# Performance work log

Measured on AMD Instinct MI355X. Metric: run time of the kernel, lower is better.

The kernel has to match this reference:

```python
import math
import jax, jax.numpy as jnp
import numpy as np

B, T, C = 4, 2048, 1024
NH, HD = 16, 64  # n_head, head_dim
RANK = 128


def setup_inputs() -> dict:
    key = jax.random.key(0)
    ks = jax.random.split(key, 9)
    s_in = 1.0 / math.sqrt(C)
    s_r = 1.0 / math.sqrt(RANK)
    inp = {"x": jax.random.normal(ks[0], (B, T, C), dtype=jnp.float32)}
    for i, name in enumerate(["q", "k", "v", "c"]):
        inp[name + "A"] = jax.random.normal(ks[1 + 2 * i], (RANK, C), dtype=jnp.float32) * s_in
        inp[name + "B"] = jax.random.normal(ks[2 + 2 * i], (C, RANK), dtype=jnp.float32) * s_r
    return inp


def _lowrank(x, A, Bf):
    # HarmonicLinear: rank-r factorized linear, W = Bf @ A, y = x @ W^T
    return (x @ A.T) @ Bf.T


def reference(x, qA, qB, kA, kB, vA, vB, cA, cB):
    b, t, c = x.shape
    q = _lowrank(x, qA, qB).reshape(b, t, NH, HD).transpose(0, 2, 1, 3)  # [b,h,t,d]
    k = _lowrank(x, kA, kB).reshape(b, t, NH, HD).transpose(0, 2, 1, 3)
    v = _lowrank(x, vA, vB).reshape(b, t, NH, HD).transpose(0, 2, 1, 3)
    att = jnp.einsum("bhqd,bhkd->bhqk", q, k) * (1.0 / math.sqrt(HD))
    causal = jnp.tril(jnp.ones((t, t), dtype=bool))
    att = jnp.where(causal, att, -jnp.inf)
    att = jax.nn.softmax(att, axis=-1)
    y = jnp.einsum("bhqk,bhkd->bhqd", att, v)
    y = y.transpose(0, 2, 1, 3).reshape(b, t, c)
    return _lowrank(y, cA, cB)
```

## Files before the change

kernel.cpp:

```cpp
#include <hip/hip_runtime.h>

typedef unsigned short u16;
typedef __attribute__((ext_vector_type(8))) short bf16x8;
typedef __attribute__((ext_vector_type(4))) float f32x4;
typedef __attribute__((ext_vector_type(16))) float f32x16;
typedef __attribute__((ext_vector_type(4))) int i32x4;

typedef const __attribute__((address_space(1))) void gvoid_t;
typedef __attribute__((address_space(3))) void svoid_t;

__device__ __forceinline__ u16 f2bf(float f) {
  unsigned u = __builtin_bit_cast(unsigned, f);
  u += 0x7fffu + ((u >> 16) & 1u);
  return (u16)(u >> 16);
}

__device__ __forceinline__ unsigned cvtpk(float a, float b) {
  unsigned r;
  asm("v_cvt_pk_bf16_f32 %0, %1, %2" : "=v"(r) : "v"(a), "v"(b));
  return r;
}

__device__ __forceinline__ void gload_lds16(const u16* g, u16* ldsbase) {
  __builtin_amdgcn_global_load_lds((gvoid_t*)g, (svoid_t*)ldsbase, 16, 0, 0);
}

__device__ __forceinline__ void mfma16(f32x4& d, bf16x8 a, bf16x8 b) {
  asm("v_mfma_f32_16x16x32_bf16 %0, %1, %2, %0" : "+v"(d) : "v"(a), "v"(b));
}
__device__ __forceinline__ void mfma32(f32x16& d, bf16x8 a, bf16x8 b) {
  asm("v_mfma_f32_32x32x16_bf16 %0, %1, %2, %0" : "+v"(d) : "v"(a), "v"(b));
}
__device__ __forceinline__ void mfma_fence4(f32x4& a, f32x4& b, f32x4& c, f32x4& d) {
  asm volatile("s_nop 7\n\ts_nop 7" : "+v"(a), "+v"(b), "+v"(c), "+v"(d));
}
__device__ __forceinline__ void fence16x2(f32x16& a, f32x16& b) {
  asm volatile("s_nop 7\n\ts_nop 7\n\ts_nop 7" : "+v"(a), "+v"(b));
}

struct W8 { const float* s[8]; };
__global__ __launch_bounds__(256) void cvt_all_kernel(const float* __restrict__ x,
                                                      W8 w, u16* __restrict__ xb,
                                                      u16* __restrict__ wb) {
  const int b = blockIdx.x;
  const float* src;
  u16* dst;
  int i;
  if (b < 8192) {
    src = x; dst = xb;
    i = (b * 256 + (int)threadIdx.x) * 4;
  } else {
    const int wi = (b - 8192) >> 7;
    const int wo = (b - 8192) & 127;
    src = w.s[wi]; dst = wb + (size_t)wi * 131072;
    i = (wo * 256 + (int)threadIdx.x) * 4;
  }
  float4 v = *(const float4*)(src + i);
  ushort4 o = {f2bf(v.x), f2bf(v.y), f2bf(v.z), f2bf(v.w)};
  *(ushort4*)(dst + i) = o;
}

struct G3 { const u16* A[3]; const u16* B[3]; void* C[3]; float osc[3]; int vt[3]; };

template <typename OutT, int BM>
__global__ __launch_bounds__(256) void gemm_nt(G3 g, int M, int N, int K) {
  constexpr int NI = (BM == 128) ? 4 : 2;
  __shared__ __align__(16) u16 At[2][BM * 64];
  __shared__ __align__(16) u16 Bt[2][128 * 64];
  const int z = blockIdx.z;
  const u16* __restrict__ A = g.A[z];
  const u16* __restrict__ Bw = g.B[z];
  const float osc = g.osc[z];
  const int tid = threadIdx.x;
  const int lane = tid & 63, w = tid >> 6;
  const int wm = (BM == 128) ? (w >> 1) : 0;
  const int wn = (BM == 128) ? (w & 1) : w;
  constexpr int WNW = (BM == 128) ? 64 : 32;
  const int l15 = lane & 15, l4 = lane >> 4;
  const int row0 = blockIdx.x * BM, col0 = blockIdx.y * 128;
  const int srow = lane >> 3;
  const int schunk = ((lane & 7) ^ srow) * 8;
  const u16* Ag = A + (size_t)(row0 + w * 8 + srow) * K + schunk;
  const u16* Bg = Bw + (size_t)(col0 + w * 8 + srow) * K + schunk;
  f32x4 acc[4][NI] = {};
  auto STAGE = [&](int k0, int buf) {
#pragma unroll
    for (int i = 0; i < BM / 32; ++i)
      gload_lds16(Ag + (size_t)i * 32 * K + k0, &At[buf][(w * 8 + i * 32) * 64]);
#pragma unroll
    for (int i = 0; i < 4; ++i)
      gload_lds16(Bg + (size_t)i * 32 * K + k0, &Bt[buf][(w * 8 + i * 32) * 64]);
  };
  STAGE(0, 0);
  asm volatile("s_waitcnt vmcnt(0)" ::: "memory");
  __syncthreads();
  const int nk = K >> 6;
  for (int t = 0; t < nk; ++t) {
    const int cur = t & 1;
    if (t + 1 < nk) STAGE((t + 1) << 6, cur ^ 1);
#pragma unroll
    for (int kk = 0; kk < 64; kk += 32) {
      bf16x8 af[4], bfr[NI];
#pragma unroll
      for (int mi = 0; mi < 4; ++mi) {
        const int r = wm * 64 + mi * 16 + l15;
        af[mi] = *(const bf16x8*)&At[cur][r * 64 + ((kk + 8 * l4) ^ ((r & 7) << 3))];
      }
#pragma unroll
      for (int ni = 0; ni < NI; ++ni) {
        const int r = wn * WNW + ni * 16 + l15;
        bfr[ni] = *(const bf16x8*)&Bt[cur][r * 64 + ((kk + 8 * l4) ^ ((r & 7) << 3))];
      }
#pragma unroll
      for (int mi = 0; mi < 4; ++mi)
#pragma unroll
        for (int ni = 0; ni < NI; ++ni) mfma16(acc[mi][ni], af[mi], bfr[ni]);
    }
    asm volatile("s_waitcnt vmcnt(0)" ::: "memory");
    __syncthreads();
  }
#pragma unroll
  for (int mi = 0; mi < 4; ++mi)
    mfma_fence4(acc[mi][0], acc[mi][NI - 1], acc[mi][0], acc[mi][NI - 1]);
  if (g.vt[z]) {
    u16* VTo = (u16*)g.C[z];
    const int bbv = row0 >> 11;
#pragma unroll
    for (int mi = 0; mi < 4; ++mi) {
      const int r = row0 + wm * 64 + mi * 16 + l4 * 4;
      const int t0 = r & 2047;
#pragma unroll
      for (int ni = 0; ni < NI; ++ni) {
        const int c = col0 + wn * WNW + ni * 16 + l15;
        ushort4 ov = {f2bf(acc[mi][ni][0] * osc), f2bf(acc[mi][ni][1] * osc),
                      f2bf(acc[mi][ni][2] * osc), f2bf(acc[mi][ni][3] * osc)};
        *(ushort4*)(VTo + ((size_t)(bbv * 1024 + c)) * 2048 + t0) = ov;
      }
    }
  } else {
    OutT* __restrict__ C = (OutT*)g.C[z];
#pragma unroll
    for (int mi = 0; mi < 4; ++mi) {
      const int r = row0 + wm * 64 + mi * 16 + l4 * 4;
#pragma unroll
      for (int ni = 0; ni < NI; ++ni) {
        const int c = col0 + wn * WNW + ni * 16 + l15;
#pragma unroll
        for (int j = 0; j < 4; ++j) {
          float v = acc[mi][ni][j] * osc;
          if constexpr (sizeof(OutT) == 2)
            ((u16*)C)[(size_t)(r + j) * N + c] = f2bf(v);
          else
            ((float*)C)[(size_t)(r + j) * N + c] = v;
        }
      }
    }
  }
}

__global__ __launch_bounds__(256, 4) void attn_kernel(const u16* __restrict__ Qg,
                                                      const u16* __restrict__ Kg,
                                                      const u16* __restrict__ VTg,
                                                      u16* __restrict__ Yg) {
  __shared__ __align__(16) u16 Kt[2][64 * 64];
  __shared__ __align__(16) u16 Vt[2][64 * 64];
  const int tid = threadIdx.x;
  const int lane = tid & 63, w = tid >> 6;
  const int l31 = lane & 31, hi = lane >> 5;
  const int f = blockIdx.x;
  const int qt = 15 - (f >> 6);
  const int bhid = f & 63;
  const int bb = bhid >> 4, h = bhid & 15;
  const size_t rb = (size_t)bb * 2048;
  const int h64 = h * 64;
  const int qb0 = qt << 7;
  const int qg = qb0 + w * 32 + l31;
  const int qend = qb0 + w * 32 + 31;
  const u16* Kbh = Kg + rb * 1024 + h64;
  const u16* VTbh = VTg + (size_t)bhid * 64 * 2048;
  const int srow = lane >> 3;
  const int schunk = ((lane & 7) ^ srow) * 8;

  bf16x8 qf[4];
#pragma unroll
  for (int kd = 0; kd < 4; ++kd)
    qf[kd] = *(const bf16x8*)(Qg + (rb + qg) * 1024 + h64 + kd * 16 + 8 * hi);

  f32x16 o0 = {}, o1 = {};
  const float MNEG = -30000.f;
  float lrun = 0.f;

  auto STAGE = [&](int it, int buf) {
    const int kv0 = it << 6;
    const int r0 = w * 16;
#pragma unroll
    for (int i = 0; i < 2; ++i) {
      gload_lds16(Kbh + (size_t)(kv0 + r0 + i * 8 + srow) * 1024 + schunk,
                  &Kt[buf][(r0 + i * 8) * 64]);
      gload_lds16(VTbh + (size_t)(r0 + i * 8 + srow) * 2048 + kv0 + schunk,
                  &Vt[buf][(r0 + i * 8) * 64]);
    }
  };
  STAGE(0, 0);
  asm volatile("s_waitcnt vmcnt(0)" ::: "memory");
  __syncthreads();

  const int nkv = 2 * qt + 2;
  for (int t = 0; t < nkv; ++t) {
    const int cur = t & 1;
    if (t + 1 < nkv) STAGE(t + 1, cur ^ 1);
    const int kv0 = t << 6;
    if (kv0 <= qend) {
      f32x16 s0 = {}, s1 = {};
      __builtin_amdgcn_s_setprio(1);
#pragma unroll
      for (int kd = 0; kd < 4; ++kd) {
        const int col = (kd * 16 + 8 * hi) ^ ((l31 & 7) << 3);
        bf16x8 kf0 = *(const bf16x8*)&Kt[cur][l31 * 64 + col];
        bf16x8 kf1 = *(const bf16x8*)&Kt[cur][(32 + l31) * 64 + col];
        mfma32(s0, kf0, qf[kd]);
        mfma32(s1, kf1, qf[kd]);
      }
      __builtin_amdgcn_s_setprio(0);
      fence16x2(s0, s1);
      if (kv0 + 63 > qb0 + w * 32) {
        const int lim = qg - (kv0 + 4 * hi);
#pragma unroll
        for (int r = 0; r < 16; ++r) {
          const int C0 = (r & 3) + 8 * (r >> 2);
          if (C0 > lim) s0[r] = MNEG;
          if (C0 + 32 > lim) s1[r] = MNEG;
        }
      }
#pragma unroll
      for (int r = 0; r < 16; ++r) {
        s0[r] = exp2f(s0[r]);
        s1[r] = exp2f(s1[r]);
      }
      float t8[8];
#pragma unroll
      for (int r = 0; r < 8; ++r)
        t8[r] = (s0[2 * r] + s0[2 * r + 1]) + (s1[2 * r] + s1[2 * r + 1]);
      float rs = ((t8[0] + t8[1]) + (t8[2] + t8[3])) +
                 ((t8[4] + t8[5]) + (t8[6] + t8[7]));
      lrun += rs + __shfl_xor(rs, 32, 64);
      i32x4 paw[4];
#pragma unroll
      for (int tl = 0; tl < 2; ++tl) {
        const f32x16& p = tl ? s1 : s0;
#pragma unroll
        for (int ks = 0; ks < 2; ++ks) {
          unsigned pk0 = cvtpk(p[8 * ks + 0], p[8 * ks + 1]);
          unsigned pk1 = cvtpk(p[8 * ks + 2], p[8 * ks + 3]);
          unsigned pk2 = cvtpk(p[8 * ks + 4], p[8 * ks + 5]);
          unsigned pk3 = cvtpk(p[8 * ks + 6], p[8 * ks + 7]);
          unsigned x0 = (unsigned)__shfl_xor((int)pk0, 32, 64);
          unsigned x1 = (unsigned)__shfl_xor((int)pk1, 32, 64);
          unsigned x2 = (unsigned)__shfl_xor((int)pk2, 32, 64);
          unsigned x3 = (unsigned)__shfl_xor((int)pk3, 32, 64);
          i32x4 A;
          A[0] = (int)(hi ? x2 : pk0);
          A[1] = (int)(hi ? x3 : pk1);
          A[2] = (int)(hi ? pk2 : x0);
          A[3] = (int)(hi ? pk3 : x1);
          paw[tl * 2 + ks] = A;
        }
      }
      asm volatile("s_nop 1");
      __builtin_amdgcn_s_setprio(1);
#pragma unroll
      for (int tl = 0; tl < 2; ++tl)
#pragma unroll
        for (int ks = 0; ks < 2; ++ks) {
          bf16x8 pa = __builtin_bit_cast(bf16x8, paw[tl * 2 + ks]);
          const int kvc = tl * 32 + ks * 16 + 8 * hi;
#pragma unroll
          for (int dt = 0; dt < 2; ++dt) {
            const int row = dt * 32 + l31;
            bf16x8 vf = *(const bf16x8*)&Vt[cur][row * 64 + (kvc ^ ((l31 & 7) << 3))];
            if (dt == 0) mfma32(o0, vf, pa);
            else         mfma32(o1, vf, pa);
          }
        }
      __builtin_amdgcn_s_setprio(0);
    }
    asm volatile("s_waitcnt vmcnt(0)" ::: "memory");
    __syncthreads();
  }
  fence16x2(o0, o1);
  const float inv = 1.f / lrun;
  u16* Yrow = Yg + (rb + qg) * 1024 + h64;
#pragma unroll
  for (int r = 0; r < 16; r += 2) {
    const int dbase = (r & 3) + 8 * (r >> 2) + 4 * hi;
    *(unsigned*)(Yrow + dbase) = cvtpk(o0[r] * inv, o0[r + 1] * inv);
    *(unsigned*)(Yrow + 32 + dbase) = cvtpk(o1[r] * inv, o1[r + 1] * inv);
  }
}

extern "C" void kernel_launch(void* const* d_in, const int* in_sizes, int n_in,
                              void* d_out, int out_size, void* d_ws, size_t ws_size,
                              hipStream_t stream) {
  const float* x = (const float*)d_in[0];
  char* ws = (char*)d_ws;
  u16* xb = (u16*)ws;
  u16* wb = (u16*)(ws + (16u << 20));
  u16* Rq = (u16*)(ws + (18u << 20));
  u16* Rk = (u16*)(ws + (20u << 20));
  u16* Rv = (u16*)(ws + (22u << 20));
  u16* Ry = (u16*)(ws + (24u << 20));
  u16* Qb = (u16*)(ws + (26u << 20));
  u16* Kb = (u16*)(ws + (42u << 20));
  u16* VT = (u16*)(ws + (58u << 20));
  const int WSZ = 131072;
  const float SC = 0.18033688011112042f;

  W8 wp;
  for (int i = 0; i < 8; ++i) wp.s[i] = (const float*)d_in[1 + i];
  cvt_all_kernel<<<8192 + 1024, 256, 0, stream>>>(x, wp, xb, wb);

  G3 g1;
  g1.A[0] = g1.A[1] = g1.A[2] = xb;
  g1.B[0] = wb; g1.B[1] = wb + 2 * WSZ; g1.B[2] = wb + 4 * WSZ;
  g1.C[0] = Rq; g1.C[1] = Rk; g1.C[2] = Rv;
  g1.osc[0] = g1.osc[1] = g1.osc[2] = 1.f;
  g1.vt[0] = g1.vt[1] = g1.vt[2] = 0;
  gemm_nt<u16, 64><<<dim3(128, 1, 3), 256, 0, stream>>>(g1, 8192, 128, 1024);

  G3 g2;
  g2.A[0] = Rq; g2.A[1] = Rk; g2.A[2] = Rv;
  g2.B[0] = wb + 1 * WSZ; g2.B[1] = wb + 3 * WSZ; g2.B[2] = wb + 5 * WSZ;
  g2.C[0] = Qb; g2.C[1] = Kb; g2.C[2] = VT;
  g2.osc[0] = SC; g2.osc[1] = 1.f; g2.osc[2] = 1.f;
  g2.vt[0] = 0; g2.vt[1] = 0; g2.vt[2] = 1;
  gemm_nt<u16, 128><<<dim3(64, 8, 3), 256, 0, stream>>>(g2, 8192, 1024, 128);

  attn_kernel<<<dim3(1024), 256, 0, stream>>>(Qb, Kb, VT, xb);

  G3 g3;
  g3.A[0] = g3.A[1] = g3.A[2] = xb;
  g3.B[0] = g3.B[1] = g3.B[2] = wb + 6 * WSZ;
  g3.C[0] = g3.C[1] = g3.C[2] = Ry;
  g3.osc[0] = g3.osc[1] = g3.osc[2] = 1.f;
  g3.vt[0] = g3.vt[1] = g3.vt[2] = 0;
  gemm_nt<u16, 64><<<dim3(128, 1, 1), 256, 0, stream>>>(g3, 8192, 128, 1024);
  G3 g4;
  g4.A[0] = g4.A[1] = g4.A[2] = Ry;
  g4.B[0] = g4.B[1] = g4.B[2] = wb + 7 * WSZ;
  g4.C[0] = g4.C[1] = g4.C[2] = d_out;
  g4.osc[0] = g4.osc[1] = g4.osc[2] = 1.f;
  g4.vt[0] = g4.vt[1] = g4.vt[2] = 0;
  gemm_nt<float, 128><<<dim3(64, 8, 1), 256, 0, stream>>>(g4, 8192, 1024, 128);
}
```

Measured before the change: 144.3 us.

## Load V fragments directly from global memory and interleave causal tile order

Removes the LDS staging buffer for V and has each lane load its V^T fragments straight from global memory into registers, issued early so they overlap the softmax. This halves LDS use, so launch bounds rise to 5 blocks per CU for higher occupancy. The block-to-query-tile mapping changes from strictly descending to an interleaved long/short ordering to balance causal work across CUs. The cost is per-wave global loads that are not shared across the block's four waves, which adds L2 traffic and latency that is only partly hidden.

```diff
diff --git a/kernel.cpp b/kernel.cpp
--- a/kernel.cpp
+++ b/kernel.cpp
@@ -158,17 +158,18 @@
   }
 }
 
-__global__ __launch_bounds__(256, 4) void attn_kernel(const u16* __restrict__ Qg,
+__global__ __launch_bounds__(256, 5) void attn_kernel(const u16* __restrict__ Qg,
                                                       const u16* __restrict__ Kg,
                                                       const u16* __restrict__ VTg,
                                                       u16* __restrict__ Yg) {
   __shared__ __align__(16) u16 Kt[2][64 * 64];
-  __shared__ __align__(16) u16 Vt[2][64 * 64];
   const int tid = threadIdx.x;
   const int lane = tid & 63, w = tid >> 6;
   const int l31 = lane & 31, hi = lane >> 5;
   const int f = blockIdx.x;
-  const int qt = 15 - (f >> 6);
+  const int s = f >> 6;
+  const int qt = (s < 4) ? 15 - 2 * s : (s < 8) ? 2 * s - 8
+               : (s < 12) ? 30 - 2 * s : 2 * s - 23;
   const int bhid = f & 63;
   const int bb = bhid >> 4, h = bhid & 15;
   const size_t rb = (size_t)bb * 2048;
@@ -178,6 +179,8 @@
   const int qend = qb0 + w * 32 + 31;
   const u16* Kbh = Kg + rb * 1024 + h64;
   const u16* VTbh = VTg + (size_t)bhid * 64 * 2048;
+  const u16* Vrow0 = VTbh + (size_t)l31 * 2048;
+  const u16* Vrow1 = VTbh + (size_t)(32 + l31) * 2048;
   const int srow = lane >> 3;
   const int schunk = ((lane & 7) ^ srow) * 8;
 
@@ -194,12 +197,9 @@
     const int kv0 = it << 6;
     const int r0 = w * 16;
 #pragma unroll
-    for (int i = 0; i < 2; ++i) {
+    for (int i = 0; i < 2; ++i)
       gload_lds16(Kbh + (size_t)(kv0 + r0 + i * 8 + srow) * 1024 + schunk,
                   &Kt[buf][(r0 + i * 8) * 64]);
-      gload_lds16(VTbh + (size_t)(r0 + i * 8 + srow) * 2048 + kv0 + schunk,
-                  &Vt[buf][(r0 + i * 8) * 64]);
-    }
   };
   STAGE(0, 0);
   asm volatile("s_waitcnt vmcnt(0)" ::: "memory");
@@ -222,6 +222,12 @@
         mfma32(s1, kf1, qf[kd]);
       }
       __builtin_amdgcn_s_setprio(0);
+      bf16x8 va[2][2];
+#pragma unroll
+      for (int ks = 0; ks < 2; ++ks) {
+        va[ks][0] = *(const bf16x8*)(Vrow0 + kv0 + ks * 16 + 8 * hi);
+        va[ks][1] = *(const bf16x8*)(Vrow1 + kv0 + ks * 16 + 8 * hi);
+      }
       fence16x2(s0, s1);
       if (kv0 + 63 > qb0 + w * 32) {
         const int lim = qg - (kv0 + 4 * hi);
@@ -266,22 +272,25 @@
           paw[tl * 2 + ks] = A;
         }
       }
-      asm volatile("s_nop 1");
+      bf16x8 vb[2][2];
+#pragma unroll
+      for (int ks = 0; ks < 2; ++ks) {
+        vb[ks][0] = *(const bf16x8*)(Vrow0 + kv0 + 32 + ks * 16 + 8 * hi);
+        vb[ks][1] = *(const bf16x8*)(Vrow1 + kv0 + 32 + ks * 16 + 8 * hi);
+      }
       __builtin_amdgcn_s_setprio(1);
 #pragma unroll
-      for (int tl = 0; tl < 2; ++tl)
-#pragma unroll
-        for (int ks = 0; ks < 2; ++ks) {
-          bf16x8 pa = __builtin_bit_cast(bf16x8, paw[tl * 2 + ks]);
-          const int kvc = tl * 32 + ks * 16 + 8 * hi;
-#pragma unroll
-          for (int dt = 0; dt < 2; ++dt) {
-            const int row = dt * 32 + l31;
-            bf16x8 vf = *(const bf16x8*)&Vt[cur][row * 64 + (kvc ^ ((l31 & 7) << 3))];
-            if (dt == 0) mfma32(o0, vf, pa);
-            else         mfma32(o1, vf, pa);
-          }
-        }
+      for (int ks = 0; ks < 2; ++ks) {
+        bf16x8 pa = __builtin_bit_cast(bf16x8, paw[ks]);
+        mfma32(o0, va[ks][0], pa);
+        mfma32(o1, va[ks][1], pa);
+      }
+#pragma unroll
+      for (int ks = 0; ks < 2; ++ks) {
+        bf16x8 pa = __builtin_bit_cast(bf16x8, paw[2 + ks]);
+        mfma32(o0, vb[ks][0], pa);
+        mfma32(o1, vb[ks][1], pa);
+      }
       __builtin_amdgcn_s_setprio(0);
     }
     asm volatile("s_waitcnt vmcnt(0)" ::: "memory");
```

Measured after the change: 288.7 us. +100.1%, slower.

## Split long causal attention tiles across KV ranges and merge partials

Applied to the files above, without the earlier changes.

Query tiles 8-15, which have the longest causal KV loops, are now each split into two blocks covering halves of the KV range, giving 1536 blocks in a reordered, more balanced schedule. The split blocks write unnormalized fp32 partial outputs and row sums to scratch, reusing the output buffer and a freed workspace region, and a new merge kernel sums them and normalizes. Launch bounds also move to 5 waves per SIMD to raise occupancy. The merge adds a kernel launch and extra global traffic, and it relies on a shared fixed max offset so that the partials can simply be added.

```diff
diff --git a/kernel.cpp b/kernel.cpp
--- a/kernel.cpp
+++ b/kernel.cpp
@@ -37,6 +37,10 @@
 __device__ __forceinline__ void fence16x2(f32x16& a, f32x16& b) {
   asm volatile("s_nop 7\n\ts_nop 7\n\ts_nop 7" : "+v"(a), "+v"(b));
 }
+
+__constant__ int cQT[24] = {7,15,15,14,14,6,13,13,12,12,5,11,11,10,10,4,9,9,8,8,3,2,1,0};
+__constant__ int cI0[24] = {0,0,16,0,15,0,0,14,0,13,0,0,12,0,11,0,0,10,0,9,0,0,0,0};
+__constant__ int cI1[24] = {16,16,32,15,30,14,14,28,13,26,12,12,24,11,22,10,10,20,9,18,8,6,4,2};
 
 struct W8 { const float* s[8]; };
 __global__ __launch_bounds__(256) void cvt_all_kernel(const float* __restrict__ x,
@@ -158,17 +162,20 @@
   }
 }
 
-__global__ __launch_bounds__(256, 4) void attn_kernel(const u16* __restrict__ Qg,
+__global__ __launch_bounds__(256, 5) void attn_kernel(const u16* __restrict__ Qg,
                                                       const u16* __restrict__ Kg,
                                                       const u16* __restrict__ VTg,
-                                                      u16* __restrict__ Yg) {
+                                                      u16* __restrict__ Yg,
+                                                      float* __restrict__ PSo,
+                                                      float* __restrict__ Ls) {
   __shared__ __align__(16) u16 Kt[2][64 * 64];
   __shared__ __align__(16) u16 Vt[2][64 * 64];
   const int tid = threadIdx.x;
   const int lane = tid & 63, w = tid >> 6;
   const int l31 = lane & 31, hi = lane >> 5;
   const int f = blockIdx.x;
-  const int qt = 15 - (f >> 6);
+  const int u = f >> 6;
+  const int qt = cQT[u], it0 = cI0[u], it1 = cI1[u];
   const int bhid = f & 63;
   const int bb = bhid >> 4, h = bhid & 15;
   const size_t rb = (size_t)bb * 2048;
@@ -201,14 +208,13 @@
                   &Vt[buf][(r0 + i * 8) * 64]);
     }
   };
-  STAGE(0, 0);
+  STAGE(it0, 0);
   asm volatile("s_waitcnt vmcnt(0)" ::: "memory");
   __syncthreads();
 
-  const int nkv = 2 * qt + 2;
-  for (int t = 0; t < nkv; ++t) {
-    const int cur = t & 1;
-    if (t + 1 < nkv) STAGE(t + 1, cur ^ 1);
+  for (int t = it0; t < it1; ++t) {
+    const int cur = (t - it0) & 1;
+    if (t + 1 < it1) STAGE(t + 1, cur ^ 1);
     const int kv0 = t << 6;
     if (kv0 <= qend) {
       f32x16 s0 = {}, s1 = {};
@@ -288,14 +294,46 @@
     __syncthreads();
   }
   fence16x2(o0, o1);
-  const float inv = 1.f / lrun;
-  u16* Yrow = Yg + (rb + qg) * 1024 + h64;
-#pragma unroll
-  for (int r = 0; r < 16; r += 2) {
-    const int dbase = (r & 3) + 8 * (r >> 2) + 4 * hi;
-    *(unsigned*)(Yrow + dbase) = cvtpk(o0[r] * inv, o0[r + 1] * inv);
-    *(unsigned*)(Yrow + 32 + dbase) = cvtpk(o1[r] * inv, o1[r + 1] * inv);
-  }
+  if (qt < 8) {
+    const float inv = 1.f / lrun;
+    u16* Yrow = Yg + (rb + qg) * 1024 + h64;
+#pragma unroll
+    for (int r = 0; r < 16; r += 2) {
+      const int dbase = (r & 3) + 8 * (r >> 2) + 4 * hi;
+      *(unsigned*)(Yrow + dbase) = cvtpk(o0[r] * inv, o0[r + 1] * inv);
+      *(unsigned*)(Yrow + 32 + dbase) = cvtpk(o1[r] * inv, o1[r + 1] * inv);
+    }
+  } else {
+    const int slot = ((((bhid << 3) | (qt - 8)) << 1) | (it0 != 0 ? 1 : 0));
+    float* Po = PSo + (size_t)slot * 8192 + (size_t)(w * 32 + l31) * 64;
+#pragma unroll
+    for (int g = 0; g < 4; ++g) {
+      float4 v0 = {o0[4 * g + 0], o0[4 * g + 1], o0[4 * g + 2], o0[4 * g + 3]};
+      float4 v1 = {o1[4 * g + 0], o1[4 * g + 1], o1[4 * g + 2], o1[4 * g + 3]};
+      *(float4*)(Po + 8 * g + 4 * hi) = v0;
+      *(float4*)(Po + 32 + 8 * g + 4 * hi) = v1;
+    }
+    if (!hi) Ls[slot * 128 + w * 32 + l31] = lrun;
+  }
+}
+
+__global__ __launch_bounds__(256) void merge_kernel(const float* __restrict__ PSo,
+                                                    const float* __restrict__ Ls,
+                                                    u16* __restrict__ Yg) {
+  const int m = blockIdx.x * 256 + threadIdx.x;
+  const int pair = m >> 11;
+  const int rem = m & 2047;
+  const int q = rem >> 4;
+  const int d0 = (rem & 15) << 2;
+  const int bhid = pair >> 3;
+  const int qt = (pair & 7) + 8;
+  const size_t s0 = (size_t)pair * 2;
+  const float4 a = *(const float4*)(PSo + s0 * 8192 + q * 64 + d0);
+  const float4 b = *(const float4*)(PSo + (s0 + 1) * 8192 + q * 64 + d0);
+  const float inv = 1.f / (Ls[s0 * 128 + q] + Ls[(s0 + 1) * 128 + q]);
+  u16* dst = Yg + ((size_t)(bhid >> 4) * 2048 + qt * 128 + q) * 1024 + (bhid & 15) * 64 + d0;
+  *(unsigned*)(dst) = cvtpk((a.x + b.x) * inv, (a.y + b.y) * inv);
+  *(unsigned*)(dst + 2) = cvtpk((a.z + b.z) * inv, (a.w + b.w) * inv);
 }
 
 extern "C" void kernel_launch(void* const* d_in, const int* in_sizes, int n_in,
@@ -312,6 +350,8 @@
   u16* Qb = (u16*)(ws + (26u << 20));
   u16* Kb = (u16*)(ws + (42u << 20));
   u16* VT = (u16*)(ws + (58u << 20));
+  float* Ls = (float*)(ws + (18u << 20));
+  float* PSo = (float*)d_out;
   const int WSZ = 131072;
   const float SC = 0.18033688011112042f;
 
@@ -335,7 +375,8 @@
   g2.vt[0] = 0; g2.vt[1] = 0; g2.vt[2] = 1;
   gemm_nt<u16, 128><<<dim3(64, 8, 3), 256, 0, stream>>>(g2, 8192, 1024, 128);
 
-  attn_kernel<<<dim3(1024), 256, 0, stream>>>(Qb, Kb, VT, xb);
+  attn_kernel<<<dim3(1536), 256, 0, stream>>>(Qb, Kb, VT, xb, PSo, Ls);
+  merge_kernel<<<dim3(4096), 256, 0, stream>>>(PSo, Ls, xb);
 
   G3 g3;
   g3.A[0] = g3.A[1] = g3.A[2] = xb;
```

Result: slower. 191.5 us (+32.7%).
